# Performance work log

Measured on AMD Instinct MI355X. Metric: run time of the kernel, lower is better.

The kernel has to match this reference:

```python
import jax, jax.numpy as jnp
import numpy as np

B, G, D = 256, 64, 20          # batch, genes per term, subsystem output dim
T3, T2, T1, T0 = 2048, 512, 128, 1  # terms per stratum, deepest first
FAN = 4                        # children per internal term (root gets all T1)
EPS = 1e-5                     # BatchNorm1d eps


def setup_inputs() -> dict:
    key = jax.random.key(0)
    ks = jax.random.split(key, 32)
    def genes(k, T):
        # binary gene perturbation states (column 3 of go_gene_strata_state)
        return (jax.random.uniform(k, (B, T, G)) < 0.5).astype(jnp.float32)
    def lin(kw, kb, T, din):
        # nn.init.uniform_(w, -0.001, 0.001) per DCellSubsystem
        W = jax.random.uniform(kw, (T, din, D), minval=-0.001, maxval=0.001)
        b = jax.random.uniform(kb, (T, D), minval=-0.001, maxval=0.001)
        return W, b
    in3, in2, in1, in0 = G, FAN * D + G, FAN * D + G, T1 * D + G
    W3, b3 = lin(ks[0], ks[1], T3, in3)
    W2, b2 = lin(ks[2], ks[3], T2, in2)
    W1, b1 = lin(ks[4], ks[5], T1, in1)
    W0, b0 = lin(ks[6], ks[7], T0, in0)
    ones = lambda T: jnp.ones((T, D), jnp.float32)
    zeros = lambda T: jnp.zeros((T, D), jnp.float32)
    hw0 = jax.random.normal(ks[8], (T0, D, 1)) * 0.1
    hb0 = jnp.zeros((T0, 1), jnp.float32)
    return {
        'genes3': genes(ks[9], T3), 'genes2': genes(ks[10], T2),
        'genes1': genes(ks[11], T1), 'genes0': genes(ks[12], T0),
        'W3': W3, 'b3': b3, 'g3': ones(T3), 'be3': zeros(T3),
        'W2': W2, 'b2': b2, 'g2': ones(T2), 'be2': zeros(T2),
        'W1': W1, 'b1': b1, 'g1': ones(T1), 'be1': zeros(T1),
        'W0': W0, 'b0': b0, 'g0': ones(T0), 'be0': zeros(T0),
        'hw0': hw0, 'hb0': hb0,
    }


def _subsystem(x, W, b, g, be):
    # Linear -> BatchNorm1d (training mode, batch stats over axis 0) -> Tanh
    z = jnp.einsum('bti,tio->bto', x, W) + b          # [B, T, D]
    mu = jnp.mean(z, axis=0)
    var = jnp.var(z, axis=0)                           # biased, as in torch BN
    zn = (z - mu) * jax.lax.rsqrt(var + EPS)
    return jnp.tanh(zn * g + be)


def reference(genes3, genes2, genes1, genes0,
              W3, b3, g3, be3, W2, b2, g2, be2,
              W1, b1, g1, be1, W0, b0, g0, be0, hw0, hb0):
    # stratum 3 (leaves): input is gene states only
    h3 = _subsystem(genes3, W3, b3, g3, be3)           # [B, T3, D]
    # stratum 2: concat FAN contiguous children + own gene states
    x2 = jnp.concatenate([h3.reshape(B, T2, FAN * D), genes2], axis=-1)
    h2 = _subsystem(x2, W2, b2, g2, be2)               # [B, T2, D]
    x1 = jnp.concatenate([h2.reshape(B, T1, FAN * D), genes1], axis=-1)
    h1 = _subsystem(x1, W1, b1, g1, be1)               # [B, T1, D]
    # root: all T1 children + root gene states
    x0 = jnp.concatenate([h1.reshape(B, T0, T1 * D), genes0], axis=-1)
    h0 = _subsystem(x0, W0, b0, g0, be0)               # [B, 1, D]
    pred = jnp.einsum('bto,toc->btc', h0, hw0) + hb0   # root linear head
    return pred.reshape(B, 1)
```

## Files before the change

kernel.cpp:

```cpp
#include <hip/hip_runtime.h>
#include <hip/hip_fp16.h>


#define DEV static __device__ __forceinline__

constexpr int B_  = 256, G_ = 64, D_ = 20;
constexpr int T3_ = 2048, T2_ = 512, T1_ = 128;
constexpr float EPS_ = 1e-5f;
constexpr int INM = 4 * D_ + G_;

constexpr size_t N_H3 = (size_t)T3_ * B_ * D_;
constexpr size_t N_H2 = (size_t)T2_ * B_ * D_;
constexpr size_t N_H1 = (size_t)B_ * T1_ * D_;
constexpr size_t OFF_H3B = 0;
constexpr size_t OFF_H2B = OFF_H3B + N_H3 * 2;
constexpr size_t OFF_H1B = OFF_H2B + N_H2 * 2;
constexpr size_t OFF_Z0B = OFF_H1B + N_H1 * 4;

constexpr int GSTRIDE_U = 33;

typedef _Float16 hf2 __attribute__((ext_vector_type(2)));

DEV float dot2f(uint xu, uint wu, float c) {
#if __has_builtin(__builtin_amdgcn_fdot2)
    return __builtin_amdgcn_fdot2(__builtin_bit_cast(hf2, xu),
                                  __builtin_bit_cast(hf2, wu), c, false);
#else
    union { uint u; __half2 h; } X, W;
    X.u = xu; W.u = wu;
    c = fmaf(__low2float(X.h),  __low2float(W.h),  c);
    return fmaf(__high2float(X.h), __high2float(W.h), c);
#endif
}

DEV float fast_tanh(float x) {
    float e = __expf(2.0f * x);
    return fmaf(-2.0f, __builtin_amdgcn_rcpf(e + 1.0f), 1.0f);
}

DEV void stage_genes(const float* __restrict__ genes_t, size_t rowStrideF,
                     uint* ldsg, int tid) {
    const int e = tid & 15, r0 = tid >> 4;
#pragma unroll
    for (int it = 0; it < 16; ++it) {
        const int row = r0 + 16 * it;
        float4 f = ((const float4*)(genes_t + (size_t)row * rowStrideF))[e];
        union { __half2 h2; uint u; } p0, p1;
        p0.h2 = __floats2half2_rn(f.x, f.y);
        p1.h2 = __floats2half2_rn(f.z, f.w);
        ldsg[GSTRIDE_U * row + 2 * e]     = p0.u;
        ldsg[GSTRIDE_U * row + 2 * e + 1] = p1.u;
    }
}

template <int NP, int DCH>
DEV void stage_weights(const float* __restrict__ Wt, int o0, uint* ldsw, int tid) {
    constexpr int NU = NP * DCH;
#pragma unroll
    for (int j0 = 0; j0 < NU; j0 += 256) {
        int j = j0 + tid;
        if (NU % 256 != 0 && j >= NU) break;
        int p = j / DCH, oo = j - p * DCH;
        float w0 = Wt[(2 * p) * D_ + o0 + oo];
        float w1 = Wt[(2 * p + 1) * D_ + o0 + oo];
        union { __half2 h2; uint u; } pk;
        pk.h2 = __floats2half2_rn(w0, w1);
        ldsw[j] = pk.u;
    }
}

template <int N>
DEV void bn_tanh(const float (&acc)[N], const float* gterm, const float* beterm,
                 int o0, int tid, float (&h)[N]) {
    __shared__ float sred[4][N], qred[4][N], Avec[N], Cvec[N];
    const int lane = tid & 63, wave = tid >> 6;
    float s[N], q[N];
#pragma unroll
    for (int o = 0; o < N; ++o) { s[o] = acc[o]; q[o] = acc[o] * acc[o]; }
#pragma unroll
    for (int off = 32; off; off >>= 1) {
#pragma unroll
        for (int o = 0; o < N; ++o) {
            s[o] += __shfl_xor(s[o], off, 64);
            q[o] += __shfl_xor(q[o], off, 64);
        }
    }
    if (lane == 0) {
#pragma unroll
        for (int o = 0; o < N; ++o) { sred[wave][o] = s[o]; qred[wave][o] = q[o]; }
    }
    __syncthreads();
    if (tid < N) {
        float S = sred[0][tid] + sred[1][tid] + sred[2][tid] + sred[3][tid];
        float Q = qred[0][tid] + qred[1][tid] + qred[2][tid] + qred[3][tid];
        float mu  = S * (1.0f / B_);
        float var = fmaxf(Q * (1.0f / B_) - mu * mu, 0.0f);
        float rstd = rsqrtf(var + EPS_);
        float A = rstd * gterm[o0 + tid];
        Avec[tid] = A;
        Cvec[tid] = beterm[o0 + tid] - mu * A;
    }
    __syncthreads();
#pragma unroll
    for (int o = 0; o < N; ++o) h[o] = fast_tanh(fmaf(acc[o], Avec[o], Cvec[o]));
}

template <int DCH>
DEV void load_wrow(const uint* ldsw, int p, uint (&w)[DCH]) {
    const uint* row = ldsw + p * DCH;
    if constexpr (DCH % 4 == 0) {
#pragma unroll
        for (int v = 0; v < DCH / 4; ++v) {
            uint4 u = ((const uint4*)row)[v];
            w[4 * v] = u.x; w[4 * v + 1] = u.y; w[4 * v + 2] = u.z; w[4 * v + 3] = u.w;
        }
    } else {
#pragma unroll
        for (int v = 0; v < DCH / 2; ++v) {
            uint2 u = ((const uint2*)row)[v];
            w[2 * v] = u.x; w[2 * v + 1] = u.y;
        }
    }
}

__global__ __launch_bounds__(256, 4) void k_stage3(const float* __restrict__ genes,
                                                   const float* __restrict__ W,
                                                   const float* __restrict__ g,
                                                   const float* __restrict__ be,
                                                   __half* __restrict__ hout) {
    __shared__ uint ldsg[B_ * GSTRIDE_U];
    __shared__ uint ldsw[(G_ / 2) * D_];
    const int t = blockIdx.x, b = threadIdx.x;
    stage_genes(genes + (size_t)t * G_, (size_t)T3_ * G_, ldsg, b);
    stage_weights<G_ / 2, D_>(W + (size_t)t * (G_ * D_), 0, ldsw, b);
    __syncthreads();
    float acc[D_] = {};
#pragma unroll
    for (int p = 0; p < G_ / 2; ++p) {
        uint xu = ldsg[GSTRIDE_U * b + p];
        uint w[D_];
        load_wrow<D_>(ldsw, p, w);
#pragma unroll
        for (int o = 0; o < D_; ++o) acc[o] = dot2f(xu, w[o], acc[o]);
    }
    float h[D_];
    bn_tanh<D_>(acc, g + (size_t)t * D_, be + (size_t)t * D_, 0, b, h);
    uint2* dst = (uint2*)(hout + ((size_t)t * B_ + b) * D_);
#pragma unroll
    for (int v = 0; v < 5; ++v) {
        union { __half2 h2[2]; uint2 u; } pk;
        pk.h2[0] = __floats2half2_rn(h[4 * v],     h[4 * v + 1]);
        pk.h2[1] = __floats2half2_rn(h[4 * v + 2], h[4 * v + 3]);
        dst[v] = pk.u;
    }
}

template <int T, int DCH, bool OUT_HALF_TERM_MAJOR>
__global__ __launch_bounds__(256, 2) void k_mid(const __half* __restrict__ hsrc,
                                                const float* __restrict__ genes,
                                                const float* __restrict__ W,
                                                const float* __restrict__ g,
                                                const float* __restrict__ be,
                                                void* __restrict__ hout_) {
    constexpr int NCH = D_ / DCH;
    constexpr int NP = INM / 2;
    __shared__ uint ldsg[B_ * GSTRIDE_U];
    __shared__ uint ldsw[NP * DCH];
    const int t = blockIdx.x / NCH, o0 = (blockIdx.x % NCH) * DCH;
    const int b = threadIdx.x;
    stage_genes(genes + (size_t)t * G_, (size_t)T * G_, ldsg, b);
    stage_weights<NP, DCH>(W + (size_t)t * (INM * D_), o0, ldsw, b);
    __syncthreads();

    float acc[DCH] = {};
#pragma unroll
    for (int c = 0; c < 4; ++c) {
        const uint2* hp = (const uint2*)(hsrc + ((size_t)(4 * t + c) * B_ + b) * D_);
        uint xc[10];
#pragma unroll
        for (int v = 0; v < 5; ++v) {
            uint2 u = hp[v];
            xc[2 * v] = u.x; xc[2 * v + 1] = u.y;
        }
#pragma unroll
        for (int v = 0; v < 10; ++v) {
            uint w[DCH];
            load_wrow<DCH>(ldsw, c * 10 + v, w);
#pragma unroll
            for (int o = 0; o < DCH; ++o) acc[o] = dot2f(xc[v], w[o], acc[o]);
        }
    }
#pragma unroll
    for (int p = 0; p < G_ / 2; ++p) {
        uint xu = ldsg[GSTRIDE_U * b + p];
        uint w[DCH];
        load_wrow<DCH>(ldsw, 40 + p, w);
#pragma unroll
        for (int o = 0; o < DCH; ++o) acc[o] = dot2f(xu, w[o], acc[o]);
    }
    float h[DCH];
    bn_tanh<DCH>(acc, g + (size_t)t * D_, be + (size_t)t * D_, o0, b, h);
    if (OUT_HALF_TERM_MAJOR) {
        __half* hout = (__half*)hout_;
        uint* dst = (uint*)(hout + ((size_t)t * B_ + b) * D_ + o0);
#pragma unroll
        for (int v = 0; v < DCH / 2; ++v) {
            union { __half2 h2; uint u; } pk;
            pk.h2 = __floats2half2_rn(h[2 * v], h[2 * v + 1]);
            dst[v] = pk.u;
        }
    } else {
        float* dst = (float*)hout_ + ((size_t)b * T + t) * D_ + o0;
#pragma unroll
        for (int o = 0; o < DCH; ++o) dst[o] = h[o];
    }
}

__global__ __launch_bounds__(256, 4) void k_stage0a(const float* __restrict__ h1,
                                                    const float* __restrict__ genes0,
                                                    const float* __restrict__ W0,
                                                    float* __restrict__ z0p) {
    const int b = blockIdx.x >> 2, s = blockIdx.x & 3, tid = threadIdx.x;
    const int kbase = 640 * s;
    const float* x = h1 + (size_t)b * (T1_ * D_);
    float acc[D_] = {};
#pragma unroll
    for (int j = 0; j < 3; ++j) {
        int kl = tid + 256 * j;
        if (kl < 640) {
            int k = kbase + kl;
            float xk = x[k];
            const float4* w = (const float4*)(W0 + (size_t)k * D_);
#pragma unroll
            for (int v = 0; v < D_ / 4; ++v) {
                float4 f = w[v];
                acc[4 * v + 0] = fmaf(xk, f.x, acc[4 * v + 0]);
                acc[4 * v + 1] = fmaf(xk, f.y, acc[4 * v + 1]);
                acc[4 * v + 2] = fmaf(xk, f.z, acc[4 * v + 2]);
                acc[4 * v + 3] = fmaf(xk, f.w, acc[4 * v + 3]);
            }
        }
    }
    if (s == 3 && tid < G_) {
        float xk = genes0[(size_t)b * G_ + tid];
        const float4* w = (const float4*)(W0 + (size_t)(T1_ * D_ + tid) * D_);
#pragma unroll
        for (int v = 0; v < D_ / 4; ++v) {
            float4 f = w[v];
            acc[4 * v + 0] = fmaf(xk, f.x, acc[4 * v + 0]);
            acc[4 * v + 1] = fmaf(xk, f.y, acc[4 * v + 1]);
            acc[4 * v + 2] = fmaf(xk, f.z, acc[4 * v + 2]);
            acc[4 * v + 3] = fmaf(xk, f.w, acc[4 * v + 3]);
        }
    }
    __shared__ float sred[4][D_];
    const int lane = tid & 63, wave = tid >> 6;
#pragma unroll
    for (int off = 32; off; off >>= 1)
#pragma unroll
        for (int o = 0; o < D_; ++o) acc[o] += __shfl_xor(acc[o], off, 64);
    if (lane == 0)
#pragma unroll
        for (int o = 0; o < D_; ++o) sred[wave][o] = acc[o];
    __syncthreads();
    if (tid < D_)
        z0p[((size_t)b * 4 + s) * D_ + tid] =
            sred[0][tid] + sred[1][tid] + sred[2][tid] + sred[3][tid];
}

__global__ __launch_bounds__(256) void k_stage0b(const float* __restrict__ z0p,
                                                 const float* __restrict__ g0,
                                                 const float* __restrict__ be0,
                                                 const float* __restrict__ hw0,
                                                 const float* __restrict__ hb0,
                                                 float* __restrict__ out) {
    const int tid = threadIdx.x;
    float acc[D_] = {};
#pragma unroll
    for (int s = 0; s < 4; ++s) {
        const float4* zp = (const float4*)(z0p + ((size_t)tid * 4 + s) * D_);
#pragma unroll
        for (int v = 0; v < D_ / 4; ++v) {
            float4 f = zp[v];
            acc[4 * v + 0] += f.x; acc[4 * v + 1] += f.y;
            acc[4 * v + 2] += f.z; acc[4 * v + 3] += f.w;
        }
    }
    float h[D_];
    bn_tanh<D_>(acc, g0, be0, 0, tid, h);
    __shared__ float hwv[D_ + 1];
    if (tid < D_) hwv[tid] = hw0[tid];
    if (tid == 0) hwv[D_] = hb0[0];
    __syncthreads();
    float pred = hwv[D_];
#pragma unroll
    for (int o = 0; o < D_; ++o) pred = fmaf(h[o], hwv[o], pred);
    out[tid] = pred;
}

extern "C" void kernel_launch(void* const* d_in, const int* in_sizes, int n_in,
                              void* d_out, int out_size, void* d_ws, size_t ws_size,
                              hipStream_t stream) {
    const float* genes3 = (const float*)d_in[0];
    const float* genes2 = (const float*)d_in[1];
    const float* genes1 = (const float*)d_in[2];
    const float* genes0 = (const float*)d_in[3];
    const float* W3  = (const float*)d_in[4];
    const float* g3  = (const float*)d_in[6];
    const float* be3 = (const float*)d_in[7];
    const float* W2  = (const float*)d_in[8];
    const float* g2  = (const float*)d_in[10];
    const float* be2 = (const float*)d_in[11];
    const float* W1  = (const float*)d_in[12];
    const float* g1  = (const float*)d_in[14];
    const float* be1 = (const float*)d_in[15];
    const float* W0  = (const float*)d_in[16];
    const float* g0  = (const float*)d_in[18];
    const float* be0 = (const float*)d_in[19];
    const float* hw0 = (const float*)d_in[20];
    const float* hb0 = (const float*)d_in[21];

    char* wsb = (char*)d_ws;
    __half* h3 = (__half*)(wsb + OFF_H3B);
    __half* h2 = (__half*)(wsb + OFF_H2B);
    float*  h1 = (float*)(wsb + OFF_H1B);
    float*  z0p = (float*)(wsb + OFF_Z0B);

    k_stage3<<<T3_, 256, 0, stream>>>(genes3, W3, g3, be3, h3);
    k_mid<T2_, 20, true ><<<T2_, 256, 0, stream>>>(h3, genes2, W2, g2, be2, h2);
    k_mid<T1_, 10, false><<<T1_ * 2, 256, 0, stream>>>(h2, genes1, W1, g1, be1, h1);
    k_stage0a<<<B_ * 4, 256, 0, stream>>>(h1, genes0, W0, z0p);
    k_stage0b<<<1, 256, 0, stream>>>(z0p, g0, be0, hw0, hb0, (float*)d_out);
}
```

Before: 330.4 us.

## Pre-transpose gene tensors to term-major fp16 and split mid stages into more blocks

Adds transpose kernels that turn each stratum's gene tensor into a term-major fp16 layout, so each thread reads its own gene row straight into registers instead of staging it through strided LDS. The gene LDS buffers are removed, the mid kernels now launch with occupancy hint 4, and the output dimension is split into more chunks (10 and 4) to raise block count. In exchange there are three extra launches and an extra full read and write of the gene data through HBM, and blocks that split outputs each reload the same inputs.

```diff
diff --git a/kernel.cpp b/kernel.cpp
--- a/kernel.cpp
+++ b/kernel.cpp
@@ -9,15 +9,19 @@
 constexpr float EPS_ = 1e-5f;
 constexpr int INM = 4 * D_ + G_;
 
-constexpr size_t N_H3 = (size_t)T3_ * B_ * D_;
-constexpr size_t N_H2 = (size_t)T2_ * B_ * D_;
-constexpr size_t N_H1 = (size_t)B_ * T1_ * D_;
-constexpr size_t OFF_H3B = 0;
-constexpr size_t OFF_H2B = OFF_H3B + N_H3 * 2;
-constexpr size_t OFF_H1B = OFF_H2B + N_H2 * 2;
-constexpr size_t OFF_Z0B = OFF_H1B + N_H1 * 4;
-
-constexpr int GSTRIDE_U = 33;
+constexpr size_t OFF_GT3 = 0;
+constexpr size_t SZ_GT3 = (size_t)T3_ * B_ * G_ * 2;
+constexpr size_t OFF_GT2 = OFF_GT3 + SZ_GT3;
+constexpr size_t SZ_GT2 = (size_t)T2_ * B_ * G_ * 2;
+constexpr size_t OFF_GT1 = OFF_GT2 + SZ_GT2;
+constexpr size_t SZ_GT1 = (size_t)T1_ * B_ * G_ * 2;
+constexpr size_t OFF_H3B = OFF_GT1 + SZ_GT1;
+constexpr size_t SZ_H3 = (size_t)T3_ * B_ * D_ * 2;
+constexpr size_t OFF_H2B = OFF_H3B + SZ_H3;
+constexpr size_t SZ_H2 = (size_t)T2_ * B_ * D_ * 2;
+constexpr size_t OFF_H1B = OFF_H2B + SZ_H2;
+constexpr size_t SZ_H1 = (size_t)B_ * T1_ * D_ * 4;
+constexpr size_t OFF_Z0B = OFF_H1B + SZ_H1;
 
 typedef _Float16 hf2 __attribute__((ext_vector_type(2)));
 
@@ -38,18 +42,33 @@
     return fmaf(-2.0f, __builtin_amdgcn_rcpf(e + 1.0f), 1.0f);
 }
 
-DEV void stage_genes(const float* __restrict__ genes_t, size_t rowStrideF,
-                     uint* ldsg, int tid) {
-    const int e = tid & 15, r0 = tid >> 4;
-#pragma unroll
-    for (int it = 0; it < 16; ++it) {
-        const int row = r0 + 16 * it;
-        float4 f = ((const float4*)(genes_t + (size_t)row * rowStrideF))[e];
-        union { __half2 h2; uint u; } p0, p1;
-        p0.h2 = __floats2half2_rn(f.x, f.y);
-        p1.h2 = __floats2half2_rn(f.z, f.w);
-        ldsg[GSTRIDE_U * row + 2 * e]     = p0.u;
-        ldsg[GSTRIDE_U * row + 2 * e + 1] = p1.u;
+template <int T>
+__global__ __launch_bounds__(256, 4) void k_transpose(const float* __restrict__ genes,
+                                                      __half* __restrict__ gT) {
+    __shared__ uint lds[64 * 4 * 33];
+    const int b0 = (blockIdx.x & 3) * 64;
+    const int t0 = (blockIdx.x >> 2) * 4;
+    const int tid = threadIdx.x, w = tid >> 6, l = tid & 63;
+#pragma unroll
+    for (int i = 0; i < 16; ++i) {
+        const int b_loc = w * 16 + i;
+        float4 f = ((const float4*)(genes + ((size_t)(b0 + b_loc) * T + t0) * G_))[l];
+        const int t = l >> 4, g4 = l & 15;
+        union { __half2 h; uint u; } a, c;
+        a.h = __floats2half2_rn(f.x, f.y);
+        c.h = __floats2half2_rn(f.z, f.w);
+        uint* row = lds + (b_loc * 4 + t) * 33;
+        row[2 * g4]     = a.u;
+        row[2 * g4 + 1] = c.u;
+    }
+    __syncthreads();
+#pragma unroll
+    for (int r = 0; r < 8; ++r) {
+        const int M = tid + 256 * r;
+        const int t = M >> 9, b = (M >> 3) & 63, u4 = M & 7;
+        const uint* row = lds + (b * 4 + t) * 33 + 4 * u4;
+        uint4 v = make_uint4(row[0], row[1], row[2], row[3]);
+        ((uint4*)(gT + (((size_t)(t0 + t) * B_) + b0 + b) * G_))[u4] = v;
     }
 }
 
@@ -69,6 +88,25 @@
     }
 }
 
+template <int DCH>
+DEV void load_wrow(const uint* ldsw, int p, uint (&w)[DCH]) {
+    const uint* row = ldsw + p * DCH;
+    if constexpr (DCH % 4 == 0) {
+#pragma unroll
+        for (int v = 0; v < DCH / 4; ++v) {
+            uint4 u = ((const uint4*)row)[v];
+            w[4 * v] = u.x; w[4 * v + 1] = u.y; w[4 * v + 2] = u.z; w[4 * v + 3] = u.w;
+        }
+    } else {
+#pragma unroll
+        for (int v = 0; v < DCH / 2; ++v) {
+            uint2 u = ((const uint2*)row)[v];
+            w[2 * v] = u.x; w[2 * v + 1] = u.y;
+        }
+        if constexpr (DCH % 2 != 0) w[DCH - 1] = row[DCH - 1];
+    }
+}
+
 template <int N>
 DEV void bn_tanh(const float (&acc)[N], const float* gterm, const float* beterm,
                  int o0, int tid, float (&h)[N]) {
@@ -105,43 +143,29 @@
     for (int o = 0; o < N; ++o) h[o] = fast_tanh(fmaf(acc[o], Avec[o], Cvec[o]));
 }
 
-template <int DCH>
-DEV void load_wrow(const uint* ldsw, int p, uint (&w)[DCH]) {
-    const uint* row = ldsw + p * DCH;
-    if constexpr (DCH % 4 == 0) {
-#pragma unroll
-        for (int v = 0; v < DCH / 4; ++v) {
-            uint4 u = ((const uint4*)row)[v];
-            w[4 * v] = u.x; w[4 * v + 1] = u.y; w[4 * v + 2] = u.z; w[4 * v + 3] = u.w;
-        }
-    } else {
-#pragma unroll
-        for (int v = 0; v < DCH / 2; ++v) {
-            uint2 u = ((const uint2*)row)[v];
-            w[2 * v] = u.x; w[2 * v + 1] = u.y;
-        }
-    }
-}
-
-__global__ __launch_bounds__(256, 4) void k_stage3(const float* __restrict__ genes,
+__global__ __launch_bounds__(256, 4) void k_stage3(const __half* __restrict__ gT,
                                                    const float* __restrict__ W,
                                                    const float* __restrict__ g,
                                                    const float* __restrict__ be,
                                                    __half* __restrict__ hout) {
-    __shared__ uint ldsg[B_ * GSTRIDE_U];
     __shared__ uint ldsw[(G_ / 2) * D_];
     const int t = blockIdx.x, b = threadIdx.x;
-    stage_genes(genes + (size_t)t * G_, (size_t)T3_ * G_, ldsg, b);
+    uint x[G_ / 2];
+    const uint4* xp = (const uint4*)(gT + ((size_t)t * B_ + b) * G_);
+#pragma unroll
+    for (int v = 0; v < G_ / 8; ++v) {
+        uint4 u = xp[v];
+        x[4 * v] = u.x; x[4 * v + 1] = u.y; x[4 * v + 2] = u.z; x[4 * v + 3] = u.w;
+    }
     stage_weights<G_ / 2, D_>(W + (size_t)t * (G_ * D_), 0, ldsw, b);
     __syncthreads();
     float acc[D_] = {};
 #pragma unroll
     for (int p = 0; p < G_ / 2; ++p) {
-        uint xu = ldsg[GSTRIDE_U * b + p];
         uint w[D_];
         load_wrow<D_>(ldsw, p, w);
 #pragma unroll
-        for (int o = 0; o < D_; ++o) acc[o] = dot2f(xu, w[o], acc[o]);
+        for (int o = 0; o < D_; ++o) acc[o] = dot2f(x[p], w[o], acc[o]);
     }
     float h[D_];
     bn_tanh<D_>(acc, g + (size_t)t * D_, be + (size_t)t * D_, 0, b, h);
@@ -156,19 +180,24 @@
 }
 
 template <int T, int DCH, bool OUT_HALF_TERM_MAJOR>
-__global__ __launch_bounds__(256, 2) void k_mid(const __half* __restrict__ hsrc,
-                                                const float* __restrict__ genes,
+__global__ __launch_bounds__(256, 4) void k_mid(const __half* __restrict__ hsrc,
+                                                const __half* __restrict__ gT,
                                                 const float* __restrict__ W,
                                                 const float* __restrict__ g,
                                                 const float* __restrict__ be,
                                                 void* __restrict__ hout_) {
     constexpr int NCH = D_ / DCH;
     constexpr int NP = INM / 2;
-    __shared__ uint ldsg[B_ * GSTRIDE_U];
     __shared__ uint ldsw[NP * DCH];
     const int t = blockIdx.x / NCH, o0 = (blockIdx.x % NCH) * DCH;
     const int b = threadIdx.x;
-    stage_genes(genes + (size_t)t * G_, (size_t)T * G_, ldsg, b);
+    uint xg[G_ / 2];
+    const uint4* xp = (const uint4*)(gT + ((size_t)t * B_ + b) * G_);
+#pragma unroll
+    for (int v = 0; v < G_ / 8; ++v) {
+        uint4 u = xp[v];
+        xg[4 * v] = u.x; xg[4 * v + 1] = u.y; xg[4 * v + 2] = u.z; xg[4 * v + 3] = u.w;
+    }
     stage_weights<NP, DCH>(W + (size_t)t * (INM * D_), o0, ldsw, b);
     __syncthreads();
 
@@ -192,11 +221,10 @@
     }
 #pragma unroll
     for (int p = 0; p < G_ / 2; ++p) {
-        uint xu = ldsg[GSTRIDE_U * b + p];
         uint w[DCH];
         load_wrow<DCH>(ldsw, 40 + p, w);
 #pragma unroll
-        for (int o = 0; o < DCH; ++o) acc[o] = dot2f(xu, w[o], acc[o]);
+        for (int o = 0; o < DCH; ++o) acc[o] = dot2f(xg[p], w[o], acc[o]);
     }
     float h[DCH];
     bn_tanh<DCH>(acc, g + (size_t)t * D_, be + (size_t)t * D_, o0, b, h);
@@ -321,14 +349,21 @@
     const float* hb0 = (const float*)d_in[21];
 
     char* wsb = (char*)d_ws;
-    __half* h3 = (__half*)(wsb + OFF_H3B);
-    __half* h2 = (__half*)(wsb + OFF_H2B);
-    float*  h1 = (float*)(wsb + OFF_H1B);
+    __half* gT3 = (__half*)(wsb + OFF_GT3);
+    __half* gT2 = (__half*)(wsb + OFF_GT2);
+    __half* gT1 = (__half*)(wsb + OFF_GT1);
+    __half* h3  = (__half*)(wsb + OFF_H3B);
+    __half* h2  = (__half*)(wsb + OFF_H2B);
+    float*  h1  = (float*)(wsb + OFF_H1B);
     float*  z0p = (float*)(wsb + OFF_Z0B);
 
-    k_stage3<<<T3_, 256, 0, stream>>>(genes3, W3, g3, be3, h3);
-    k_mid<T2_, 20, true ><<<T2_, 256, 0, stream>>>(h3, genes2, W2, g2, be2, h2);
-    k_mid<T1_, 10, false><<<T1_ * 2, 256, 0, stream>>>(h2, genes1, W1, g1, be1, h1);
+    k_transpose<T3_><<<T3_, 256, 0, stream>>>(genes3, gT3);
+    k_transpose<T2_><<<T2_, 256, 0, stream>>>(genes2, gT2);
+    k_transpose<T1_><<<T1_, 256, 0, stream>>>(genes1, gT1);
+
+    k_stage3<<<T3_, 256, 0, stream>>>(gT3, W3, g3, be3, h3);
+    k_mid<T2_, 10, true ><<<T2_ * 2, 256, 0, stream>>>(h3, gT2, W2, g2, be2, h2);
+    k_mid<T1_, 4,  false><<<T1_ * 5, 256, 0, stream>>>(h2, gT1, W1, g1, be1, h1);
     k_stage0a<<<B_ * 4, 256, 0, stream>>>(h1, genes0, W0, z0p);
     k_stage0b<<<1, 256, 0, stream>>>(z0p, g0, be0, hw0, hb0, (float*)d_out);
 }
```

Result: slower. 378.8 us (+14.6%).
